# Optimization experiments

Hardware: AMD Instinct MI355X
Metric: run time of the kernel (lower is better)

The kernel has to match this reference:

```python
import jax, jax.numpy as jnp
import numpy as np

N = 50000        # num nodes
NFEAT = 512      # input feature dim
NCLASS = 256     # output classes (out_features of out_att)
E_RAND = 800000  # random edges; + N self-loops
NEG_SLOPE = 0.2  # leakyrelu alpha


def setup_inputs() -> dict:
    key = jax.random.key(0)
    k1, k2, k3, k4 = jax.random.split(key, 4)
    x = jax.random.normal(k1, (N, NFEAT), dtype=jnp.float32)
    W = jax.random.normal(k2, (NFEAT, NCLASS), dtype=jnp.float32) / np.float32(np.sqrt(NFEAT))
    a = jax.random.normal(k3, (2 * NCLASS,), dtype=jnp.float32) / np.float32(np.sqrt(2 * NCLASS))
    rand_edges = jax.random.randint(k4, (2, E_RAND), 0, N, dtype=jnp.int32)
    self_loops = jnp.tile(jnp.arange(N, dtype=jnp.int32), (2, 1))
    edge_index = jnp.concatenate([rand_edges, self_loops], axis=1)  # [2, E]
    return {"x": x, "W": W, "a": a, "edge_index": edge_index}


def reference(x, W, a, edge_index):
    # Eval-mode SpGAT: dropout is identity (training=False).
    row, col = edge_index[0], edge_index[1]  # edge = adj.nonzero().t(): row aggregates from col
    h = x @ W                                # [N, F]
    F_out = h.shape[1]
    # a @ cat(h[row], h[col]) == (h @ a1)[row] + (h @ a2)[col]  (avoids [E, 2F] concat)
    s_row = h @ a[:F_out]                    # [N]
    s_col = h @ a[F_out:]                    # [N]
    logits = s_row[row] + s_col[col]         # [E]
    e = jnp.exp(-jax.nn.leaky_relu(logits, negative_slope=NEG_SLOPE))  # [E]
    rowsum = jax.ops.segment_sum(e, row, num_segments=N)               # [N]
    msgs = e[:, None] * h[col]                                         # [E, F]
    h_prime = jax.ops.segment_sum(msgs, row, num_segments=N) / rowsum[:, None]
    return jax.nn.log_softmax(jax.nn.elu(h_prime), axis=1)
```

## Files before the change

### kernel.cpp

```cpp
#include <hip/hip_runtime.h>
#include <math.h>

#define NNODES   50000
#define NFEAT    512
#define NCLASS   256
#define NEG_SLOPE 0.2f
#define GBLK     1564
#define BCAP     64

typedef __attribute__((ext_vector_type(8))) short short8;
typedef __attribute__((ext_vector_type(4))) float floatx4;

__device__ __forceinline__ unsigned short f2bf(float f) {
    unsigned u = __builtin_bit_cast(unsigned, f);
    u += 0x7fffu + ((u >> 16) & 1u);
    return (unsigned short)(u >> 16);
}
__device__ __forceinline__ float bf2f_lo(unsigned u) {
    return __builtin_bit_cast(float, u << 16);
}
__device__ __forceinline__ float bf2f_hi(unsigned u) {
    return __builtin_bit_cast(float, u & 0xffff0000u);
}
__device__ __forceinline__ unsigned pack_bf16_rh(float lo, float hi) {
    const unsigned ulo = __builtin_bit_cast(unsigned, lo) + 0x8000u;
    const unsigned uhi = __builtin_bit_cast(unsigned, hi) + 0x8000u;
    return __builtin_amdgcn_perm(uhi, ulo, 0x07060302);
}

#if __has_builtin(__builtin_amdgcn_fdot2_f32_bf16)
#define HAVE_DOT2 1
typedef __attribute__((ext_vector_type(2))) __bf16 bfx2;
__device__ __forceinline__ float dot2bf(unsigned hpair, unsigned epair, float acc) {
    return __builtin_amdgcn_fdot2_f32_bf16(__builtin_bit_cast(bfx2, hpair),
                                           __builtin_bit_cast(bfx2, epair), acc, false);
}
#endif

__global__ __launch_bounds__(256) void init_kernel(const float* __restrict__ W,
                                                   unsigned short* __restrict__ Wt,
                                                   int* __restrict__ cursor, int zn) {
    const int i = blockIdx.x * 256 + threadIdx.x;
    const int n = i >> 9;
    const int k = i & 511;
    Wt[i] = f2bf(W[(size_t)k * NCLASS + n]);
    if (i < zn) cursor[i] = 0;
}

__global__ __launch_bounds__(256, 4) void gemm_mfma_kernel(const float* __restrict__ x,
                                                           const unsigned short* __restrict__ Wt,
                                                           unsigned short* __restrict__ hb,
                                                           const float* __restrict__ a,
                                                           float* __restrict__ s_row,
                                                           float* __restrict__ s_col,
                                                           int M) {
    __shared__ union {
        struct { short As[2][32 * 32]; short Bs[2][256 * 32]; } k;
        short Cs[32 * 260];
    } u;

    const int tid  = threadIdx.x;
    const int w    = tid >> 6;
    const int lane = tid & 63;
    const int rowbase = blockIdx.x * 32;

    const int fm = lane & 15;
    const int fq = lane >> 4;

    floatx4 acc[2][4];
#pragma unroll
    for (int i = 0; i < 2; ++i)
#pragma unroll
        for (int j = 0; j < 4; ++j)
            acc[i][j] = (floatx4){0.f, 0.f, 0.f, 0.f};

    const int srowA = lane >> 3;
    const int skqA  = (lane & 7) << 2;
    const int arow  = min(rowbase + w * 8 + srowA, M - 1);
    const size_t abase = (size_t)arow * NFEAT + skqA;
    const int lrowA = (w * 8 + srowA) * 32 + skqA;

    const int srowB = lane >> 2;
    const int skqB  = (lane & 3) << 3;
#define STAGE_B(buf, k0)                                                                      \
    {                                                                                         \
        _Pragma("unroll")                                                                     \
        for (int t = 0; t < 4; ++t) {                                                         \
            const int seg = w * 4 + t;                                                        \
            const int nr  = seg * 16 + srowB;                                                 \
            __builtin_amdgcn_global_load_lds(                                                 \
                (const __attribute__((address_space(1))) void*)(Wt + (size_t)nr * NFEAT + (k0) + skqB), \
                (__attribute__((address_space(3))) void*)(&u.k.Bs[buf][seg * 512]), 16, 0, 0); \
        }                                                                                     \
    }

    STAGE_B(0, 0)
    {
        const float4 u0 = *(const float4*)&x[abase];
        uint2 o;
        o.x = pack_bf16_rh(u0.x, u0.y);
        o.y = pack_bf16_rh(u0.z, u0.w);
        *(uint2*)&u.k.As[0][lrowA] = o;
    }
    __syncthreads();

    int cur = 0;
    for (int k0 = 0; k0 < NFEAT; k0 += 32) {
        const int nxt = cur ^ 1;
        const bool have_next = (k0 + 32) < NFEAT;
        float4 p0;
        if (have_next) {
            p0 = *(const float4*)&x[abase + k0 + 32];
            STAGE_B(nxt, k0 + 32)
        }

        short8 af[2];
#pragma unroll
        for (int mt = 0; mt < 2; ++mt)
            af[mt] = *(const short8*)&u.k.As[cur][(mt * 16 + fm) * 32 + fq * 8];
#pragma unroll
        for (int nt = 0; nt < 4; ++nt) {
            const short8 bfr = *(const short8*)&u.k.Bs[cur][(w * 64 + nt * 16 + fm) * 32 + fq * 8];
            acc[0][nt] = __builtin_amdgcn_mfma_f32_16x16x32_bf16(af[0], bfr, acc[0][nt], 0, 0, 0);
            acc[1][nt] = __builtin_amdgcn_mfma_f32_16x16x32_bf16(af[1], bfr, acc[1][nt], 0, 0, 0);
        }

        if (have_next) {
            uint2 o;
            o.x = pack_bf16_rh(p0.x, p0.y);
            o.y = pack_bf16_rh(p0.z, p0.w);
            *(uint2*)&u.k.As[nxt][lrowA] = o;
        }
        __syncthreads();
        cur = nxt;
    }

    __syncthreads();
#pragma unroll
    for (int mt = 0; mt < 2; ++mt)
#pragma unroll
        for (int nt = 0; nt < 4; ++nt)
#pragma unroll
            for (int r = 0; r < 4; ++r)
                u.Cs[(mt * 16 + fq * 4 + r) * 260 + w * 64 + nt * 16 + fm] =
                    (short)f2bf(acc[mt][nt][r]);
    __syncthreads();
#pragma unroll
    for (int kk = 0; kk < 8; ++kk) {
        const int idx = tid + kk * 256;
        const int lrow = idx >> 6;
        const int c4 = (idx & 63) << 2;
        const int grow = rowbase + lrow;
        const uint2 vv = *(const uint2*)&u.Cs[lrow * 260 + c4];
        const float f0 = bf2f_lo(vv.x), f1 = bf2f_hi(vv.x);
        const float f2 = bf2f_lo(vv.y), f3 = bf2f_hi(vv.y);
        const float4 A1 = *(const float4*)&a[c4];
        const float4 A2 = *(const float4*)&a[NCLASS + c4];
        float p1 = f0 * A1.x + f1 * A1.y + f2 * A1.z + f3 * A1.w;
        float p2 = f0 * A2.x + f1 * A2.y + f2 * A2.z + f3 * A2.w;
#pragma unroll
        for (int off = 1; off < 64; off <<= 1) {
            p1 += __shfl_xor(p1, off);
            p2 += __shfl_xor(p2, off);
        }
        if (grow < M) {
            *(uint2*)&hb[(size_t)grow * NCLASS + c4] = vv;
            if (lane == 0) {
                s_row[grow] = p1;
                s_col[grow] = p2;
            }
        }
    }
}

__global__ __launch_bounds__(256) void scatter_kernel(const int* __restrict__ row,
                                                      const int* __restrict__ col,
                                                      int* __restrict__ cursor,
                                                      int* __restrict__ bucket, int e) {
    const int i = blockIdx.x * 256 + threadIdx.x;
    if (i >= e) return;
    const int r = row[i];
    const int c = col[i];
    const int pos = atomicAdd(&cursor[r], 1);
    if (pos < BCAP) bucket[((size_t)r << 6) + pos] = c;
}

__global__ __launch_bounds__(256) void aggregate_kernel(const unsigned short* __restrict__ hb,
                                                        const int* __restrict__ bucket,
                                                        const int* __restrict__ cnt,
                                                        const float* __restrict__ s_row,
                                                        const float* __restrict__ s_col,
                                                        float* __restrict__ out, int n) {
    const int wave = (int)((blockIdx.x * (size_t)blockDim.x + threadIdx.x) >> 6);
    const int lane = threadIdx.x & 63;
    if (wave >= n) return;
    const int r = wave;
    const int jb = r << 6;
    const int je = jb + min(cnt[r], BCAP);
    const int fo = lane << 2;
    const float sr = s_row[r];

    float rowsum = 0.f;
    int j = jb;

#define EDGE_E(c) ({ const float _l = sr + s_col[c];                         \
                     const float _lr = _l > 0.f ? _l : NEG_SLOPE * _l;       \
                     __expf(-_lr); })

#ifdef HAVE_DOT2
    float ac0 = 0.f, ac1 = 0.f, ac2 = 0.f, ac3 = 0.f;
    for (; j + 3 < je; j += 4) {
        const int4 cv = *(const int4*)&bucket[j];
        const uint2 g0 = *(const uint2*)&hb[(size_t)cv.x * NCLASS + fo];
        const uint2 g1 = *(const uint2*)&hb[(size_t)cv.y * NCLASS + fo];
        const uint2 g2 = *(const uint2*)&hb[(size_t)cv.z * NCLASS + fo];
        const uint2 g3 = *(const uint2*)&hb[(size_t)cv.w * NCLASS + fo];
        const float e0 = EDGE_E(cv.x);
        const float e1 = EDGE_E(cv.y);
        const float e2 = EDGE_E(cv.z);
        const float e3 = EDGE_E(cv.w);
        const unsigned ep01 = pack_bf16_rh(e0, e1);
        const unsigned ep23 = pack_bf16_rh(e2, e3);
        rowsum += (e0 + e1) + (e2 + e3);
        ac0 = dot2bf(__builtin_amdgcn_perm(g1.x, g0.x, 0x05040100), ep01, ac0);
        ac1 = dot2bf(__builtin_amdgcn_perm(g1.x, g0.x, 0x07060302), ep01, ac1);
        ac2 = dot2bf(__builtin_amdgcn_perm(g1.y, g0.y, 0x05040100), ep01, ac2);
        ac3 = dot2bf(__builtin_amdgcn_perm(g1.y, g0.y, 0x07060302), ep01, ac3);
        ac0 = dot2bf(__builtin_amdgcn_perm(g3.x, g2.x, 0x05040100), ep23, ac0);
        ac1 = dot2bf(__builtin_amdgcn_perm(g3.x, g2.x, 0x07060302), ep23, ac1);
        ac2 = dot2bf(__builtin_amdgcn_perm(g3.y, g2.y, 0x05040100), ep23, ac2);
        ac3 = dot2bf(__builtin_amdgcn_perm(g3.y, g2.y, 0x07060302), ep23, ac3);
    }
    float4 acc = make_float4(ac0, ac1, ac2, ac3);
#else
    float4 acc = make_float4(0.f, 0.f, 0.f, 0.f);
    for (; j + 3 < je; j += 4) {
        const int4 cv = *(const int4*)&bucket[j];
        const uint2 g0 = *(const uint2*)&hb[(size_t)cv.x * NCLASS + fo];
        const uint2 g1 = *(const uint2*)&hb[(size_t)cv.y * NCLASS + fo];
        const uint2 g2 = *(const uint2*)&hb[(size_t)cv.z * NCLASS + fo];
        const uint2 g3 = *(const uint2*)&hb[(size_t)cv.w * NCLASS + fo];
        const float e0 = EDGE_E(cv.x);
        const float e1 = EDGE_E(cv.y);
        const float e2 = EDGE_E(cv.z);
        const float e3 = EDGE_E(cv.w);
        rowsum += (e0 + e1) + (e2 + e3);
        acc.x += e0 * bf2f_lo(g0.x) + e1 * bf2f_lo(g1.x) + e2 * bf2f_lo(g2.x) + e3 * bf2f_lo(g3.x);
        acc.y += e0 * bf2f_hi(g0.x) + e1 * bf2f_hi(g1.x) + e2 * bf2f_hi(g2.x) + e3 * bf2f_hi(g3.x);
        acc.z += e0 * bf2f_lo(g0.y) + e1 * bf2f_lo(g1.y) + e2 * bf2f_lo(g2.y) + e3 * bf2f_lo(g3.y);
        acc.w += e0 * bf2f_hi(g0.y) + e1 * bf2f_hi(g1.y) + e2 * bf2f_hi(g2.y) + e3 * bf2f_hi(g3.y);
    }
#endif
    for (; j < je; ++j) {
        const int c = bucket[j];
        const uint2 g = *(const uint2*)&hb[(size_t)c * NCLASS + fo];
        const float e = EDGE_E(c);
        rowsum += e;
        acc.x += e * bf2f_lo(g.x);
        acc.y += e * bf2f_hi(g.x);
        acc.z += e * bf2f_lo(g.y);
        acc.w += e * bf2f_hi(g.y);
    }

    const float inv = 1.f / rowsum;
    float v[4] = {acc.x * inv, acc.y * inv, acc.z * inv, acc.w * inv};
#pragma unroll
    for (int i = 0; i < 4; ++i)
        v[i] = v[i] > 0.f ? v[i] : __expf(v[i]) - 1.f;

    float m = fmaxf(fmaxf(v[0], v[1]), fmaxf(v[2], v[3]));
#pragma unroll
    for (int off = 32; off > 0; off >>= 1) m = fmaxf(m, __shfl_xor(m, off));
    float s = 0.f;
#pragma unroll
    for (int i = 0; i < 4; ++i) s += __expf(v[i] - m);
#pragma unroll
    for (int off = 32; off > 0; off >>= 1) s += __shfl_xor(s, off);
    const float lse = m + __logf(s);

    float4 o = make_float4(v[0] - lse, v[1] - lse, v[2] - lse, v[3] - lse);
    *(float4*)&out[(size_t)r * NCLASS + fo] = o;
}

extern "C" void kernel_launch(void* const* d_in, const int* in_sizes, int n_in,
                              void* d_out, int out_size, void* d_ws, size_t ws_size,
                              hipStream_t stream) {
    const float* x  = (const float*)d_in[0];
    const float* W  = (const float*)d_in[1];
    const float* a  = (const float*)d_in[2];
    const int* edge = (const int*)d_in[3];
    float* out = (float*)d_out;

    const int M = in_sizes[0] / NFEAT;
    const int E = in_sizes[3] / 2;
    const int* row = edge;
    const int* col = edge + E;

    char* ws = (char*)d_ws;
    size_t off = 0;
    auto carve = [&](size_t bytes) -> char* {
        char* p = ws + off;
        off = (off + bytes + 255) & ~(size_t)255;
        return p;
    };
    unsigned short* Wt = (unsigned short*)carve((size_t)NCLASS * NFEAT * sizeof(short));
    unsigned short* hb = (unsigned short*)carve((size_t)M * NCLASS * sizeof(short));
    int*   cursor   = (int*)carve((size_t)M * sizeof(int));
    float* s_row    = (float*)carve((size_t)M * sizeof(float));
    float* s_col    = (float*)carve((size_t)M * sizeof(float));
    int*   bucket   = (int*)carve((size_t)M * BCAP * sizeof(int));

    init_kernel<<<512, 256, 0, stream>>>(W, Wt, cursor, M);

    gemm_mfma_kernel<<<GBLK, 256, 0, stream>>>(x, Wt, hb, a, s_row, s_col, M);

    scatter_kernel<<<(E + 255) / 256, 256, 0, stream>>>(row, col, cursor, bucket, E);

    aggregate_kernel<<<(M + 3) / 4, 256, 0, stream>>>(hb, bucket, cursor, s_row, s_col, out, M);
}
```

Baseline: 314.1 us.

## Preload A fragments into registers and widen GEMM tile to 64 rows

The GEMM block now covers 64 rows instead of 32. Each wave keeps its 16 rows of x for the full K=512 as bf16 MFMA fragments in registers, which removes the A tile staging through LDS. Each wave computes all 256 output columns for its rows, so every B tile loaded from LDS is reused across more rows and the number of blocks that reload W is halved. The cost is much higher register pressure (16 A fragments plus 16 accumulators), which lowers occupancy to 2 blocks per SIMD. All x loads are also issued up front, with no software prefetch overlapping them with the MFMA work.

```diff
diff --git a/kernel.cpp b/kernel.cpp
--- a/kernel.cpp
+++ b/kernel.cpp
@@ -5,7 +5,7 @@
 #define NFEAT    512
 #define NCLASS   256
 #define NEG_SLOPE 0.2f
-#define GBLK     1564
+#define GBLK     782
 #define BCAP     64
 
 typedef __attribute__((ext_vector_type(8))) short short8;
@@ -47,7 +47,7 @@
     if (i < zn) cursor[i] = 0;
 }
 
-__global__ __launch_bounds__(256, 4) void gemm_mfma_kernel(const float* __restrict__ x,
+__global__ __launch_bounds__(256, 2) void gemm_mfma_kernel(const float* __restrict__ x,
                                                            const unsigned short* __restrict__ Wt,
                                                            unsigned short* __restrict__ hb,
                                                            const float* __restrict__ a,
@@ -55,119 +55,105 @@
                                                            float* __restrict__ s_col,
                                                            int M) {
     __shared__ union {
-        struct { short As[2][32 * 32]; short Bs[2][256 * 32]; } k;
+        short Bs[2][256 * 32];
         short Cs[32 * 260];
     } u;
 
     const int tid  = threadIdx.x;
     const int w    = tid >> 6;
     const int lane = tid & 63;
-    const int rowbase = blockIdx.x * 32;
+    const int rowbase = blockIdx.x * 64;
 
     const int fm = lane & 15;
     const int fq = lane >> 4;
 
-    floatx4 acc[2][4];
-#pragma unroll
-    for (int i = 0; i < 2; ++i)
-#pragma unroll
-        for (int j = 0; j < 4; ++j)
-            acc[i][j] = (floatx4){0.f, 0.f, 0.f, 0.f};
-
-    const int srowA = lane >> 3;
-    const int skqA  = (lane & 7) << 2;
-    const int arow  = min(rowbase + w * 8 + srowA, M - 1);
-    const size_t abase = (size_t)arow * NFEAT + skqA;
-    const int lrowA = (w * 8 + srowA) * 32 + skqA;
-
-    const int srowB = lane >> 2;
-    const int skqB  = (lane & 3) << 3;
+    const int arow = min(rowbase + w * 16 + fm, M - 1);
+    const float* xrow = x + (size_t)arow * NFEAT + fq * 8;
+    short8 af[16];
+#pragma unroll
+    for (int kk = 0; kk < 16; ++kk) {
+        const float4 a0 = *(const float4*)(xrow + kk * 32);
+        const float4 a1 = *(const float4*)(xrow + kk * 32 + 4);
+        uint4 o;
+        o.x = pack_bf16_rh(a0.x, a0.y);
+        o.y = pack_bf16_rh(a0.z, a0.w);
+        o.z = pack_bf16_rh(a1.x, a1.y);
+        o.w = pack_bf16_rh(a1.z, a1.w);
+        af[kk] = __builtin_bit_cast(short8, o);
+    }
+
+    floatx4 acc[16];
+#pragma unroll
+    for (int nt = 0; nt < 16; ++nt)
+        acc[nt] = (floatx4){0.f, 0.f, 0.f, 0.f};
+
+    const int srow = lane >> 2;
+    const int skq  = (lane & 3) << 3;
 #define STAGE_B(buf, k0)                                                                      \
     {                                                                                         \
         _Pragma("unroll")                                                                     \
         for (int t = 0; t < 4; ++t) {                                                         \
             const int seg = w * 4 + t;                                                        \
-            const int nr  = seg * 16 + srowB;                                                 \
+            const int nr  = seg * 16 + srow;                                                  \
             __builtin_amdgcn_global_load_lds(                                                 \
-                (const __attribute__((address_space(1))) void*)(Wt + (size_t)nr * NFEAT + (k0) + skqB), \
-                (__attribute__((address_space(3))) void*)(&u.k.Bs[buf][seg * 512]), 16, 0, 0); \
+                (const __attribute__((address_space(1))) void*)(Wt + (size_t)nr * NFEAT + (k0) + skq), \
+                (__attribute__((address_space(3))) void*)(&u.Bs[buf][seg * 512]), 16, 0, 0);  \
         }                                                                                     \
     }
 
     STAGE_B(0, 0)
-    {
-        const float4 u0 = *(const float4*)&x[abase];
-        uint2 o;
-        o.x = pack_bf16_rh(u0.x, u0.y);
-        o.y = pack_bf16_rh(u0.z, u0.w);
-        *(uint2*)&u.k.As[0][lrowA] = o;
-    }
     __syncthreads();
 
-    int cur = 0;
-    for (int k0 = 0; k0 < NFEAT; k0 += 32) {
-        const int nxt = cur ^ 1;
-        const bool have_next = (k0 + 32) < NFEAT;
-        float4 p0;
-        if (have_next) {
-            p0 = *(const float4*)&x[abase + k0 + 32];
-            STAGE_B(nxt, k0 + 32)
+#pragma unroll
+    for (int kk = 0; kk < 16; ++kk) {
+        const int cur = kk & 1;
+        if (kk < 15) {
+            STAGE_B(cur ^ 1, (kk + 1) * 32)
         }
-
-        short8 af[2];
-#pragma unroll
-        for (int mt = 0; mt < 2; ++mt)
-            af[mt] = *(const short8*)&u.k.As[cur][(mt * 16 + fm) * 32 + fq * 8];
-#pragma unroll
-        for (int nt = 0; nt < 4; ++nt) {
-            const short8 bfr = *(const short8*)&u.k.Bs[cur][(w * 64 + nt * 16 + fm) * 32 + fq * 8];
-            acc[0][nt] = __builtin_amdgcn_mfma_f32_16x16x32_bf16(af[0], bfr, acc[0][nt], 0, 0, 0);
-            acc[1][nt] = __builtin_amdgcn_mfma_f32_16x16x32_bf16(af[1], bfr, acc[1][nt], 0, 0, 0);
-        }
-
-        if (have_next) {
-            uint2 o;
-            o.x = pack_bf16_rh(p0.x, p0.y);
-            o.y = pack_bf16_rh(p0.z, p0.w);
-            *(uint2*)&u.k.As[nxt][lrowA] = o;
+#pragma unroll
+        for (int nt = 0; nt < 16; ++nt) {
+            const short8 bfr = *(const short8*)&u.Bs[cur][(nt * 16 + fm) * 32 + fq * 8];
+            acc[nt] = __builtin_amdgcn_mfma_f32_16x16x32_bf16(af[kk], bfr, acc[nt], 0, 0, 0);
         }
         __syncthreads();
-        cur = nxt;
-    }
-
-    __syncthreads();
-#pragma unroll
-    for (int mt = 0; mt < 2; ++mt)
-#pragma unroll
-        for (int nt = 0; nt < 4; ++nt)
-#pragma unroll
-            for (int r = 0; r < 4; ++r)
-                u.Cs[(mt * 16 + fq * 4 + r) * 260 + w * 64 + nt * 16 + fm] =
-                    (short)f2bf(acc[mt][nt][r]);
-    __syncthreads();
-#pragma unroll
-    for (int kk = 0; kk < 8; ++kk) {
-        const int idx = tid + kk * 256;
-        const int lrow = idx >> 6;
-        const int c4 = (idx & 63) << 2;
-        const int grow = rowbase + lrow;
-        const uint2 vv = *(const uint2*)&u.Cs[lrow * 260 + c4];
-        const float f0 = bf2f_lo(vv.x), f1 = bf2f_hi(vv.x);
-        const float f2 = bf2f_lo(vv.y), f3 = bf2f_hi(vv.y);
-        const float4 A1 = *(const float4*)&a[c4];
-        const float4 A2 = *(const float4*)&a[NCLASS + c4];
-        float p1 = f0 * A1.x + f1 * A1.y + f2 * A1.z + f3 * A1.w;
-        float p2 = f0 * A2.x + f1 * A2.y + f2 * A2.z + f3 * A2.w;
-#pragma unroll
-        for (int off = 1; off < 64; off <<= 1) {
-            p1 += __shfl_xor(p1, off);
-            p2 += __shfl_xor(p2, off);
+    }
+
+#pragma unroll
+    for (int p = 0; p < 2; ++p) {
+        __syncthreads();
+        if ((w >> 1) == p) {
+            const int wr = (w & 1) * 16;
+#pragma unroll
+            for (int nt = 0; nt < 16; ++nt)
+#pragma unroll
+                for (int r = 0; r < 4; ++r)
+                    u.Cs[(wr + fq * 4 + r) * 260 + nt * 16 + fm] = (short)f2bf(acc[nt][r]);
         }
-        if (grow < M) {
-            *(uint2*)&hb[(size_t)grow * NCLASS + c4] = vv;
-            if (lane == 0) {
-                s_row[grow] = p1;
-                s_col[grow] = p2;
+        __syncthreads();
+#pragma unroll
+        for (int kk = 0; kk < 8; ++kk) {
+            const int idx = tid + kk * 256;
+            const int lrow = idx >> 6;
+            const int c4 = (idx & 63) << 2;
+            const int grow = rowbase + p * 32 + lrow;
+            const uint2 vv = *(const uint2*)&u.Cs[lrow * 260 + c4];
+            const float f0 = bf2f_lo(vv.x), f1 = bf2f_hi(vv.x);
+            const float f2 = bf2f_lo(vv.y), f3 = bf2f_hi(vv.y);
+            const float4 A1 = *(const float4*)&a[c4];
+            const float4 A2 = *(const float4*)&a[NCLASS + c4];
+            float p1 = f0 * A1.x + f1 * A1.y + f2 * A1.z + f3 * A1.w;
+            float p2 = f0 * A2.x + f1 * A2.y + f2 * A2.z + f3 * A2.w;
+#pragma unroll
+            for (int off = 1; off < 64; off <<= 1) {
+                p1 += __shfl_xor(p1, off);
+                p2 += __shfl_xor(p2, off);
+            }
+            if (grow < M) {
+                *(uint2*)&hb[(size_t)grow * NCLASS + c4] = vv;
+                if (lane == 0) {
+                    s_row[grow] = p1;
+                    s_col[grow] = p2;
+                }
             }
         }
     }
```

After: 310.6 us. Within noise of the previous version (-1.1%).
